# Kernel optimization log

Hardware: AMD Instinct MI355X
Metric: run time of the kernel (lower is better)

Reference implementation:

```python
import jax, jax.numpy as jnp
import numpy as np


def setup_inputs() -> dict:
    key = jax.random.key(0)
    k1, k2, k3 = jax.random.split(key, 3)
    B, N, C = 16, 596, 768
    x = jax.random.normal(k1, (B, N, C), dtype=jnp.float32)
    w_qkv = jax.random.normal(k2, (C, 3 * C), dtype=jnp.float32) * (C ** -0.5)
    b_qkv = jnp.zeros((3 * C,), dtype=jnp.float32)
    w_proj = jax.random.normal(k3, (C, C), dtype=jnp.float32) * (C ** -0.5)
    b_proj = jnp.zeros((C,), dtype=jnp.float32)
    return {"x": x, "w_qkv": w_qkv, "b_qkv": b_qkv, "w_proj": w_proj,
            "b_proj": b_proj, "num_heads": 12, "num_cls": 20}


def reference(x, w_qkv, b_qkv, w_proj, b_proj, num_heads, num_cls):
    B, N, C = x.shape
    H = num_heads
    Dh = C // H
    scale = Dh ** -0.5
    # qkv projection -> (3, B, H, N, Dh)
    qkv = (x @ w_qkv + b_qkv).reshape(B, N, 3, H, Dh).transpose(2, 0, 3, 1, 4)
    q, k, v = qkv[0], qkv[1], qkv[2]
    # raw scores (B, H, N, N)
    attn = jnp.einsum('bhqd,bhkd->bhqk', q, k) * scale
    # dual-group softmax: cls columns and patch columns normalized separately
    attn_cls = jax.nn.softmax(attn[..., :num_cls], axis=-1)
    attn_pat = jax.nn.softmax(attn[..., num_cls:], axis=-1)
    attn = jnp.concatenate((attn_cls, attn_pat), axis=-1)
    weights = attn
    out = jnp.einsum('bhqk,bhkd->bhqd', attn, v)
    out = out.transpose(0, 2, 1, 3).reshape(B, N, C)
    out = out @ w_proj + b_proj
    return out, weights
```

## Files before the change

kernel.cpp:

```cpp
#include <hip/hip_runtime.h>
#include <hip/hip_fp16.h>
#include <stdint.h>

typedef _Float16 f16;
typedef _Float16 f16x8 __attribute__((ext_vector_type(8)));
typedef _Float16 f16x4 __attribute__((ext_vector_type(4)));
typedef float f32x4 __attribute__((ext_vector_type(4)));

#define MFMA16(a, b, c) __builtin_amdgcn_mfma_f32_16x16x32_f16(a, b, c, 0, 0, 0)

constexpr int BB   = 16;
constexpr int NN   = 596;
constexpr int CC   = 768;
constexpr int HH   = 12;
constexpr int DH   = 64;
constexpr int NCLS = 20;
constexpr int BH   = BB * HH;
constexpr int NP   = 608;
constexpr int NPQ  = 640;
constexpr int MM   = BB * NN;
constexpr int MMP  = 9600;
constexpr int K3C  = 3 * CC;
constexpr int NT   = NP / 16;
constexpr int TPW  = 10;
constexpr int NQT  = NPQ / 64;
constexpr int NWG64 = NQT * BH;

#define QSCALE 0.18033688011112042f

__device__ __forceinline__ void gload16(const f16* g, f16* l) {
  __builtin_amdgcn_global_load_lds(
      (const __attribute__((address_space(1))) void*)g,
      (__attribute__((address_space(3))) void*)l, 16, 0, 0);
}

__global__ __launch_bounds__(256) void prep(
    const float* __restrict__ w_qkv, const float* __restrict__ w_proj,
    const float* __restrict__ x, f16* __restrict__ wqkvT,
    f16* __restrict__ wprojT, f16* __restrict__ x16, f16* __restrict__ q,
    f16* __restrict__ k, f16* __restrict__ vT) {
  __shared__ float t[32][33];
  int b = blockIdx.x;
  if (b < 1728 + 576) {
    const float* src = b < 1728 ? w_qkv : w_proj;
    f16* dst = b < 1728 ? wqkvT : wprojT;
    int Ccols = b < 1728 ? K3C : CC;
    int bi = b < 1728 ? b : b - 1728;
    int nbx = Ccols / 32;
    int tile_c = (bi % nbx) * 32, tile_r = (bi / nbx) * 32;
    int tr = threadIdx.x & 31, tg = threadIdx.x >> 5;
#pragma unroll
    for (int i = 0; i < 4; i++)
      t[tg + i * 8][tr] = src[(size_t)(tile_r + tg + i * 8) * Ccols + tile_c + tr];
    __syncthreads();
#pragma unroll
    for (int i = 0; i < 4; i++)
      dst[(size_t)(tile_c + tg + i * 8) * CC + tile_r + tr] =
          (f16)t[tr][tg + i * 8];
    return;
  }
  b -= 1728 + 576;
  if (b < 3600) {
    size_t idx = ((size_t)b * 256 + threadIdx.x) * 8;
    f16x8 h;
    if (idx < (size_t)MM * CC) {
      float4 v0 = *reinterpret_cast<const float4*>(&x[idx]);
      float4 v1 = *reinterpret_cast<const float4*>(&x[idx + 4]);
      h[0] = (f16)v0.x; h[1] = (f16)v0.y; h[2] = (f16)v0.z; h[3] = (f16)v0.w;
      h[4] = (f16)v1.x; h[5] = (f16)v1.y; h[6] = (f16)v1.z; h[7] = (f16)v1.w;
    } else {
      h = (f16x8){0, 0, 0, 0, 0, 0, 0, 0};
    }
    *reinterpret_cast<f16x8*>(&x16[idx]) = h;
    return;
  }
  b -= 3600;
  int tid = threadIdx.x;
  for (int i = tid; i < (NPQ - NN) * DH; i += 256) {
    int n = NN + (i >> 6), d = i & 63;
    q[((size_t)b * NPQ + n) * DH + d] = (f16)0.f;
  }
  for (int i = tid; i < 12 * DH; i += 256) {
    int n = NN + (i >> 6), d = i & 63;
    k[((size_t)b * NP + n) * DH + d] = (f16)0.f;
  }
  for (int i = tid; i < DH * 12; i += 256) {
    int d = i / 12, n = NN + (i % 12);
    vT[((size_t)b * DH + d) * NP + n] = (f16)0.f;
  }
}

__global__ __launch_bounds__(256) void qkv_gemm(
    const f16* __restrict__ x16, const f16* __restrict__ wT,
    const float* __restrict__ bias, f16* __restrict__ q,
    f16* __restrict__ karr, f16* __restrict__ vT) {
  __shared__ f16 sbuf[128 * 132];
  f16* As = sbuf;
  f16* Bs = sbuf + 128 * 64;
  int bn = blockIdx.x, bm = blockIdx.y;
  int tid = threadIdx.x;
  int wid = tid >> 6, lane = tid & 63;
  int wm = wid >> 1, wn = wid & 1;
  int lr = lane & 15, lg = lane >> 4;
  int srcChunk = (lane & 7) ^ (lane >> 3);

  const f16* gA = &x16[((size_t)bm * 128 + (lane >> 3)) * CC + srcChunk * 8];
  const f16* gB = &wT[((size_t)bn * 128 + (lane >> 3)) * CC + srcChunk * 8];

  f32x4 acc[4][4] = {};
  for (int k0 = 0; k0 < CC; k0 += 64) {
#pragma unroll
    for (int j = 0; j < 4; j++) {
      int r0 = (wid * 4 + j) * 8;
      gload16(gA + (size_t)r0 * CC + k0, &As[r0 * 64]);
      gload16(gB + (size_t)r0 * CC + k0, &Bs[r0 * 64]);
    }
    __syncthreads();
#pragma unroll
    for (int ks = 0; ks < 2; ks++) {
      f16x8 a[4], b[4];
#pragma unroll
      for (int mt = 0; mt < 4; mt++)
        a[mt] = *reinterpret_cast<const f16x8*>(
            &As[(wm * 64 + mt * 16 + lr) * 64 + ((ks * 4 + lg) ^ (lr & 7)) * 8]);
#pragma unroll
      for (int nt = 0; nt < 4; nt++)
        b[nt] = *reinterpret_cast<const f16x8*>(
            &Bs[(wn * 64 + nt * 16 + lr) * 64 + ((ks * 4 + lg) ^ (lr & 7)) * 8]);
#pragma unroll
      for (int mt = 0; mt < 4; mt++)
#pragma unroll
        for (int nt = 0; nt < 4; nt++)
          acc[mt][nt] = MFMA16(a[mt], b[nt], acc[mt][nt]);
    }
    __syncthreads();
  }

  int which = bn / 6;
  int hbase = (bn % 6) * 128;

  if (which < 2) {
    float sc = (which == 0) ? QSCALE : 1.0f;
#pragma unroll
    for (int mt = 0; mt < 4; mt++)
#pragma unroll
      for (int nt = 0; nt < 4; nt++) {
        int colL = wn * 64 + nt * 16 + lr;
        float bi = bias[bn * 128 + colL];
#pragma unroll
        for (int i = 0; i < 4; i++) {
          int row = wm * 64 + mt * 16 + lg * 4 + i;
          int c = colL ^ ((row & 7) << 3);
          sbuf[row * 128 + c] = (f16)((acc[mt][nt][i] + bi) * sc);
        }
      }
    __syncthreads();
#pragma unroll
    for (int p = 0; p < 8; p++) {
      int row = p * 16 + (tid >> 4);
      int c8 = tid & 15;
      int m = bm * 128 + row;
      if (m < MM) {
        f16x8 v = *reinterpret_cast<const f16x8*>(
            &sbuf[row * 128 + ((c8 ^ (row & 7)) * 8)]);
        int hcol = hbase + c8 * 8;
        int h = hcol >> 6, dc = hcol & 63;
        int b = m / NN, n = m - b * NN;
        size_t bh = (size_t)b * HH + h;
        f16* dst = (which == 0) ? &q[(bh * NPQ + n) * DH + dc]
                                : &karr[(bh * NP + n) * DH + dc];
        *reinterpret_cast<f16x8*>(dst) = v;
      }
    }
  } else {
#pragma unroll
    for (int mt = 0; mt < 4; mt++)
#pragma unroll
      for (int nt = 0; nt < 4; nt++) {
        int colL = wn * 64 + nt * 16 + lr;
        float bi = bias[bn * 128 + colL];
#pragma unroll
        for (int i = 0; i < 4; i++) {
          int row = wm * 64 + mt * 16 + lg * 4 + i;
          sbuf[colL * 132 + row] = (f16)(acc[mt][nt][i] + bi);
        }
      }
    __syncthreads();
    int nchunk = tid & 31;
    int cgrp = tid >> 5;
    int m0 = bm * 128 + nchunk * 4;
    if (m0 < MM) {
      int b = m0 / NN, n = m0 - b * NN;
#pragma unroll
      for (int it = 0; it < 16; it++) {
        int c = it * 8 + cgrp;
        f16x4 v = *reinterpret_cast<const f16x4*>(&sbuf[c * 132 + nchunk * 4]);
        int hcol = hbase + c;
        int h = hcol >> 6, dcol = hcol & 63;
        *reinterpret_cast<f16x4*>(
            &vT[((size_t)(b * HH + h) * DH + dcol) * NP + n]) = v;
      }
    }
  }
}

__global__ __launch_bounds__(256) void attn_kernel(
    const f16* __restrict__ q, const f16* __restrict__ karr,
    const f16* __restrict__ vT, float* __restrict__ weights,
    f16* __restrict__ ctx) {
  __shared__ f16 P[4][16][616];
  __shared__ float redS[4][4][16];
  __shared__ float invA_lds[4][16];
  __shared__ float invB_lds[4][16];

  int bid = blockIdx.x;
  int wgid = (bid & 7) * (NWG64 / 8) + (bid >> 3);
  int bh = wgid / NQT, qt = wgid - bh * NQT;

  int tid = threadIdx.x, wid = tid >> 6, lane = tid & 63;
  int lr = lane & 15, lg = lane >> 4;
  int qbase = qt * 64;

  const f16* qr0 = q + ((size_t)bh * NPQ + qbase + lr) * DH;
  f16x8 a[4][2];
#pragma unroll
  for (int g = 0; g < 4; g++) {
    a[g][0] = *reinterpret_cast<const f16x8*>(&qr0[g * 16 * DH + lg * 8]);
    a[g][1] = *reinterpret_cast<const f16x8*>(&qr0[g * 16 * DH + 32 + lg * 8]);
  }

  const f16* kb = karr + (size_t)bh * NP * DH;
  float psA[4] = {0.f, 0.f, 0.f, 0.f}, psB[4] = {0.f, 0.f, 0.f, 0.f};
#pragma unroll
  for (int t = 0; t < TPW; t++) {
    int ct = wid * TPW + t;
    int ctc = ct < NT ? ct : NT - 1;
    bool live = ct < NT;
    const f16* krp = &kb[(size_t)(ctc * 16 + lr) * DH];
    f16x8 b0 = *reinterpret_cast<const f16x8*>(&krp[lg * 8]);
    f16x8 b1 = *reinterpret_cast<const f16x8*>(&krp[32 + lg * 8]);
#pragma unroll
    for (int g = 0; g < 4; g++) {
      f32x4 acc = {};
      acc = MFMA16(b0, a[g][0], acc);
      acc = MFMA16(b1, a[g][1], acc);
      f16x4 pk;
#pragma unroll
      for (int i = 0; i < 4; i++) {
        int col = ct * 16 + lg * 4 + i;
        bool inA = col < NCLS;
        bool valid = live && (col < NN);
        float e = valid ? __builtin_amdgcn_exp2f(acc[i]) : 0.f;
        if (inA) psA[g] += e; else psB[g] += e;
        pk[i] = (f16)e;
      }
      if (live)
        *reinterpret_cast<f16x4*>(&P[g][lr][ct * 16 + lg * 4]) = pk;
    }
  }
#pragma unroll
  for (int g = 0; g < 4; g++) {
    psA[g] += __shfl_xor(psA[g], 16); psA[g] += __shfl_xor(psA[g], 32);
    psB[g] += __shfl_xor(psB[g], 16); psB[g] += __shfl_xor(psB[g], 32);
  }
  if (lane < 16) {
#pragma unroll
    for (int g = 0; g < 4; g++) redS[g][wid][lr] = psB[g];
    if (wid == 0)
#pragma unroll
      for (int g = 0; g < 4; g++) invA_lds[g][lr] = 1.0f / psA[g];
  }
  __syncthreads();
  if (wid == 2 && lane < 16)
#pragma unroll
    for (int g = 0; g < 4; g++)
      invB_lds[g][lr] = 1.0f / (redS[g][0][lr] + redS[g][1][lr] +
                                redS[g][2][lr] + redS[g][3][lr]);
  __syncthreads();

  {
    int row = tid >> 4, sub = tid & 15;
#pragma unroll
    for (int g = 0; g < 4; g++) {
      int grow = qbase + g * 16 + row;
      if (grow < NN) {
        float iA = invA_lds[g][row];
        float iB = invB_lds[g][row];
        const f16* prow = &P[g][row][0];
        float* wrow = weights + ((size_t)bh * NN + grow) * NN;
#pragma unroll
        for (int k2 = 0; k2 < 10; k2++) {
          int f4 = sub + 16 * k2;
          if (f4 < NN / 4) {
            float inv = (f4 < 5) ? iA : iB;
            f16x4 pv = *reinterpret_cast<const f16x4*>(&prow[f4 * 4]);
            float4 o4 = {(float)pv[0] * inv, (float)pv[1] * inv,
                         (float)pv[2] * inv, (float)pv[3] * inv};
            *reinterpret_cast<float4*>(&wrow[f4 * 4]) = o4;
          }
        }
      }
    }
  }

  const f16* vrow = vT + (size_t)bh * DH * NP + (size_t)(wid * 16 + lr) * NP;
  f32x4 oA[4] = {}, oB[4] = {};
  {
    f16x8 bv = *reinterpret_cast<const f16x8*>(&vrow[lg * 8]);
#pragma unroll
    for (int g = 0; g < 4; g++) {
      f16x8 pa = *reinterpret_cast<const f16x8*>(&P[g][lr][lg * 8]);
      f16x8 paA = pa, paB = pa;
#pragma unroll
      for (int j = 0; j < 8; j++) {
        if (lg * 8 + j < NCLS) paB[j] = (f16)0.f;
        else paA[j] = (f16)0.f;
      }
      oA[g] = MFMA16(bv, paA, oA[g]);
      oB[g] = MFMA16(bv, paB, oB[g]);
    }
  }
#pragma unroll
  for (int j = 1; j < 19; j++) {
    f16x8 bv = *reinterpret_cast<const f16x8*>(&vrow[j * 32 + lg * 8]);
#pragma unroll
    for (int g = 0; g < 4; g++) {
      f16x8 pa = *reinterpret_cast<const f16x8*>(&P[g][lr][j * 32 + lg * 8]);
      oB[g] = MFMA16(bv, pa, oB[g]);
    }
  }

  int b = bh / HH, h = bh - b * HH;
#pragma unroll
  for (int g = 0; g < 4; g++) {
    int qrow = qbase + g * 16 + lr;
    if (qrow < NN) {
      float iA = invA_lds[g][lr], iB = invB_lds[g][lr];
      f16x4 o4;
#pragma unroll
      for (int i = 0; i < 4; i++) o4[i] = (f16)(oA[g][i] * iA + oB[g][i] * iB);
      *reinterpret_cast<f16x4*>(
          &ctx[((size_t)b * NN + qrow) * CC + h * DH + wid * 16 + lg * 4]) = o4;
    }
  }
}

__global__ __launch_bounds__(256) void proj_gemm(
    const f16* __restrict__ ctx, const f16* __restrict__ wT,
    const float* __restrict__ bias, float* __restrict__ out) {
  __shared__ f16 sbuf[128 * 128];
  f16* As = sbuf;
  f16* Bs = sbuf + 128 * 64;
  int bn = blockIdx.x, bm = blockIdx.y;
  int tid = threadIdx.x;
  int wid = tid >> 6, lane = tid & 63;
  int wm = wid >> 1, wn = wid & 1;
  int lr = lane & 15, lg = lane >> 4;
  int srcChunk = (lane & 7) ^ (lane >> 3);

  const f16* gA = &ctx[((size_t)bm * 128 + (lane >> 3)) * CC + srcChunk * 8];
  const f16* gB = &wT[((size_t)bn * 128 + (lane >> 3)) * CC + srcChunk * 8];

  f32x4 acc[4][4] = {};
  for (int k0 = 0; k0 < CC; k0 += 64) {
#pragma unroll
    for (int j = 0; j < 4; j++) {
      int r0 = (wid * 4 + j) * 8;
      gload16(gA + (size_t)r0 * CC + k0, &As[r0 * 64]);
      gload16(gB + (size_t)r0 * CC + k0, &Bs[r0 * 64]);
    }
    __syncthreads();
#pragma unroll
    for (int ks = 0; ks < 2; ks++) {
      f16x8 a[4], b[4];
#pragma unroll
      for (int mt = 0; mt < 4; mt++)
        a[mt] = *reinterpret_cast<const f16x8*>(
            &As[(wm * 64 + mt * 16 + lr) * 64 + ((ks * 4 + lg) ^ (lr & 7)) * 8]);
#pragma unroll
      for (int nt = 0; nt < 4; nt++)
        b[nt] = *reinterpret_cast<const f16x8*>(
            &Bs[(wn * 64 + nt * 16 + lr) * 64 + ((ks * 4 + lg) ^ (lr & 7)) * 8]);
#pragma unroll
      for (int mt = 0; mt < 4; mt++)
#pragma unroll
        for (int nt = 0; nt < 4; nt++)
          acc[mt][nt] = MFMA16(a[mt], b[nt], acc[mt][nt]);
    }
    __syncthreads();
  }

  float* fbuf = (float*)sbuf;
#pragma unroll
  for (int pass = 0; pass < 2; pass++) {
    if (pass) __syncthreads();
    if (wm == pass) {
#pragma unroll
      for (int mt = 0; mt < 4; mt++)
#pragma unroll
        for (int nt = 0; nt < 4; nt++) {
          int colL = wn * 64 + nt * 16 + lr;
          float bi = bias[bn * 128 + colL];
#pragma unroll
          for (int i = 0; i < 4; i++) {
            int row = mt * 16 + lg * 4 + i;
            fbuf[row * 128 + colL] = acc[mt][nt][i] + bi;
          }
        }
    }
    __syncthreads();
    int f4 = tid & 31, rg2 = tid >> 5;
#pragma unroll
    for (int it = 0; it < 8; it++) {
      int row = it * 8 + rg2;
      int m = bm * 128 + pass * 64 + row;
      if (m < MM) {
        float4 v = *reinterpret_cast<const float4*>(&fbuf[row * 128 + f4 * 4]);
        *reinterpret_cast<float4*>(
            &out[(size_t)m * CC + bn * 128 + f4 * 4]) = v;
      }
    }
  }
}

extern "C" void kernel_launch(void* const* d_in, const int* in_sizes, int n_in,
                              void* d_out, int out_size, void* d_ws,
                              size_t ws_size, hipStream_t stream) {
  const float* x      = (const float*)d_in[0];
  const float* w_qkv  = (const float*)d_in[1];
  const float* b_qkv  = (const float*)d_in[2];
  const float* w_proj = (const float*)d_in[3];
  const float* b_proj = (const float*)d_in[4];

  float* out     = (float*)d_out;
  float* weights = out + (size_t)MM * CC;

  f16* p      = (f16*)d_ws;
  f16* wqkvT  = p;  p += (size_t)K3C * CC;
  f16* wprojT = p;  p += (size_t)CC * CC;
  f16* x16    = p;  p += (size_t)MMP * CC;
  f16* qb     = p;  p += (size_t)BH * NPQ * DH;
  f16* kb     = p;  p += (size_t)BH * NP * DH;
  f16* vT     = p;  p += (size_t)BH * DH * NP;
  f16* ctx    = p;  p += (size_t)MMP * CC;

  prep<<<1728 + 576 + 3600 + 192, 256, 0, stream>>>(w_qkv, w_proj, x, wqkvT,
                                                    wprojT, x16, qb, kb, vT);
  qkv_gemm<<<dim3(K3C / 128, MMP / 128), 256, 0, stream>>>(x16, wqkvT, b_qkv,
                                                           qb, kb, vT);
  attn_kernel<<<NWG64, 256, 0, stream>>>(qb, kb, vT, weights, ctx);
  proj_gemm<<<dim3(CC / 128, MMP / 128), 256, 0, stream>>>(ctx, wprojT, b_proj,
                                                           out);
}
```

Measured before the change: 183.4 us.

## Recompute QK scores in a second pass to write normalized weights directly

The attention kernel now makes a first QK^T pass that only accumulates the two group-wise exp sums, then a second pass that recomputes the scores, normalizes them, and writes fp32 weights straight from registers while storing normalized fp16 P to LDS. This removes the separate LDS-read pass for the weights output and the split cls/patch accumulators in the PV MMA, which now uses one pre-normalized accumulator. The cost is doubling the QK MFMAs and exp evaluations, plus weight stores in the MFMA fragment layout, which may coalesce worse than the previous row-contiguous write loop.

```diff
diff --git a/kernel.cpp b/kernel.cpp
--- a/kernel.cpp
+++ b/kernel.cpp
@@ -230,12 +230,70 @@
   }
 
   const f16* kb = karr + (size_t)bh * NP * DH;
+
   float psA[4] = {0.f, 0.f, 0.f, 0.f}, psB[4] = {0.f, 0.f, 0.f, 0.f};
+#pragma unroll
+  for (int t = 0; t < TPW; t++) {
+    int ct = wid * TPW + t;
+    int ctc = ct < NT ? ct : NT - 1;
+    int c0 = ct * 16 + lg * 4;
+    bool colok = (ct < NT) && (c0 < NN);
+    bool inA = c0 < NCLS;
+    const f16* krp = &kb[(size_t)(ctc * 16 + lr) * DH];
+    f16x8 b0 = *reinterpret_cast<const f16x8*>(&krp[lg * 8]);
+    f16x8 b1 = *reinterpret_cast<const f16x8*>(&krp[32 + lg * 8]);
+#pragma unroll
+    for (int g = 0; g < 4; g++) {
+      f32x4 acc = {};
+      acc = MFMA16(b0, a[g][0], acc);
+      acc = MFMA16(b1, a[g][1], acc);
+      float s = 0.f;
+#pragma unroll
+      for (int i = 0; i < 4; i++)
+        s += colok ? __builtin_amdgcn_exp2f(acc[i]) : 0.f;
+      if (inA) psA[g] += s; else psB[g] += s;
+    }
+  }
+#pragma unroll
+  for (int g = 0; g < 4; g++) {
+    psA[g] += __shfl_xor(psA[g], 16); psA[g] += __shfl_xor(psA[g], 32);
+    psB[g] += __shfl_xor(psB[g], 16); psB[g] += __shfl_xor(psB[g], 32);
+  }
+  if (lane < 16) {
+#pragma unroll
+    for (int g = 0; g < 4; g++) redS[g][wid][lr] = psB[g];
+    if (wid == 0)
+#pragma unroll
+      for (int g = 0; g < 4; g++) invA_lds[g][lr] = 1.0f / psA[g];
+  }
+  __syncthreads();
+  if (wid == 2 && lane < 16)
+#pragma unroll
+    for (int g = 0; g < 4; g++)
+      invB_lds[g][lr] = 1.0f / (redS[g][0][lr] + redS[g][1][lr] +
+                                redS[g][2][lr] + redS[g][3][lr]);
+  __syncthreads();
+
+  float iA[4], iB[4];
+  float* wbase[4];
+  bool rowok[4];
+#pragma unroll
+  for (int g = 0; g < 4; g++) {
+    iA[g] = invA_lds[g][lr];
+    iB[g] = invB_lds[g][lr];
+    int qrow = qbase + g * 16 + lr;
+    rowok[g] = qrow < NN;
+    wbase[g] = weights + ((size_t)bh * NN + qrow) * NN;
+  }
+
 #pragma unroll
   for (int t = 0; t < TPW; t++) {
     int ct = wid * TPW + t;
     int ctc = ct < NT ? ct : NT - 1;
     bool live = ct < NT;
+    int c0 = ct * 16 + lg * 4;
+    bool colok = live && (c0 < NN);
+    bool inA = c0 < NCLS;
     const f16* krp = &kb[(size_t)(ctc * 16 + lr) * DH];
     f16x8 b0 = *reinterpret_cast<const f16x8*>(&krp[lg * 8]);
     f16x8 b1 = *reinterpret_cast<const f16x8*>(&krp[32 + lg * 8]);
@@ -244,89 +302,33 @@
       f32x4 acc = {};
       acc = MFMA16(b0, a[g][0], acc);
       acc = MFMA16(b1, a[g][1], acc);
+      float inv_ = inA ? iA[g] : iB[g];
       f16x4 pk;
+      f32x4 w4;
 #pragma unroll
       for (int i = 0; i < 4; i++) {
-        int col = ct * 16 + lg * 4 + i;
-        bool inA = col < NCLS;
-        bool valid = live && (col < NN);
-        float e = valid ? __builtin_amdgcn_exp2f(acc[i]) : 0.f;
-        if (inA) psA[g] += e; else psB[g] += e;
-        pk[i] = (f16)e;
+        float e = colok ? __builtin_amdgcn_exp2f(acc[i]) : 0.f;
+        float w = e * inv_;
+        pk[i] = (f16)w;
+        w4[i] = w;
       }
       if (live)
-        *reinterpret_cast<f16x4*>(&P[g][lr][ct * 16 + lg * 4]) = pk;
-    }
-  }
-#pragma unroll
-  for (int g = 0; g < 4; g++) {
-    psA[g] += __shfl_xor(psA[g], 16); psA[g] += __shfl_xor(psA[g], 32);
-    psB[g] += __shfl_xor(psB[g], 16); psB[g] += __shfl_xor(psB[g], 32);
-  }
-  if (lane < 16) {
-#pragma unroll
-    for (int g = 0; g < 4; g++) redS[g][wid][lr] = psB[g];
-    if (wid == 0)
-#pragma unroll
-      for (int g = 0; g < 4; g++) invA_lds[g][lr] = 1.0f / psA[g];
+        *reinterpret_cast<f16x4*>(&P[g][lr][c0]) = pk;
+      if (colok && rowok[g])
+        *reinterpret_cast<f32x4*>(&wbase[g][c0]) = w4;
+    }
   }
   __syncthreads();
-  if (wid == 2 && lane < 16)
-#pragma unroll
-    for (int g = 0; g < 4; g++)
-      invB_lds[g][lr] = 1.0f / (redS[g][0][lr] + redS[g][1][lr] +
-                                redS[g][2][lr] + redS[g][3][lr]);
-  __syncthreads();
-
-  {
-    int row = tid >> 4, sub = tid & 15;
-#pragma unroll
-    for (int g = 0; g < 4; g++) {
-      int grow = qbase + g * 16 + row;
-      if (grow < NN) {
-        float iA = invA_lds[g][row];
-        float iB = invB_lds[g][row];
-        const f16* prow = &P[g][row][0];
-        float* wrow = weights + ((size_t)bh * NN + grow) * NN;
-#pragma unroll
-        for (int k2 = 0; k2 < 10; k2++) {
-          int f4 = sub + 16 * k2;
-          if (f4 < NN / 4) {
-            float inv = (f4 < 5) ? iA : iB;
-            f16x4 pv = *reinterpret_cast<const f16x4*>(&prow[f4 * 4]);
-            float4 o4 = {(float)pv[0] * inv, (float)pv[1] * inv,
-                         (float)pv[2] * inv, (float)pv[3] * inv};
-            *reinterpret_cast<float4*>(&wrow[f4 * 4]) = o4;
-          }
-        }
-      }
-    }
-  }
 
   const f16* vrow = vT + (size_t)bh * DH * NP + (size_t)(wid * 16 + lr) * NP;
-  f32x4 oA[4] = {}, oB[4] = {};
-  {
-    f16x8 bv = *reinterpret_cast<const f16x8*>(&vrow[lg * 8]);
-#pragma unroll
-    for (int g = 0; g < 4; g++) {
-      f16x8 pa = *reinterpret_cast<const f16x8*>(&P[g][lr][lg * 8]);
-      f16x8 paA = pa, paB = pa;
-#pragma unroll
-      for (int j = 0; j < 8; j++) {
-        if (lg * 8 + j < NCLS) paB[j] = (f16)0.f;
-        else paA[j] = (f16)0.f;
-      }
-      oA[g] = MFMA16(bv, paA, oA[g]);
-      oB[g] = MFMA16(bv, paB, oB[g]);
-    }
-  }
-#pragma unroll
-  for (int j = 1; j < 19; j++) {
+  f32x4 o[4] = {};
+#pragma unroll
+  for (int j = 0; j < 19; j++) {
     f16x8 bv = *reinterpret_cast<const f16x8*>(&vrow[j * 32 + lg * 8]);
 #pragma unroll
     for (int g = 0; g < 4; g++) {
       f16x8 pa = *reinterpret_cast<const f16x8*>(&P[g][lr][j * 32 + lg * 8]);
-      oB[g] = MFMA16(bv, pa, oB[g]);
+      o[g] = MFMA16(bv, pa, o[g]);
     }
   }
 
@@ -335,10 +337,9 @@
   for (int g = 0; g < 4; g++) {
     int qrow = qbase + g * 16 + lr;
     if (qrow < NN) {
-      float iA = invA_lds[g][lr], iB = invB_lds[g][lr];
       f16x4 o4;
 #pragma unroll
-      for (int i = 0; i < 4; i++) o4[i] = (f16)(oA[g][i] * iA + oB[g][i] * iB);
+      for (int i = 0; i < 4; i++) o4[i] = (f16)o[g][i];
       *reinterpret_cast<f16x4*>(
           &ctx[((size_t)b * NN + qrow) * CC + h * DH + wid * 16 + lg * 4]) = o4;
     }
```

New measurement: 254.8 us, median of 3. +38.9%, slower.
